# Performance work log

Measured on AMD Instinct MI355X. Metric: run time of the kernel, lower is better.

## Reference

```python
import jax, jax.numpy as jnp
import numpy as np

B, T, D, H = 256, 256, 384, 64  # batch, seq (BLOCK_SIZE), D_MODEL, HEAD_SIZE


def setup_inputs() -> dict:
    key = jax.random.key(0)
    k1, k2, k3, k4 = jax.random.split(key, 4)
    x = jax.random.normal(k1, (B, T, D), dtype=jnp.float32)
    # nn.Linear(D, H, bias=False): weight [H, D]; we store transposed [D, H] for x @ W
    Wq = jax.random.normal(k2, (D, H), dtype=jnp.float32) * (1.0 / np.sqrt(D))
    Wk = jax.random.normal(k3, (D, H), dtype=jnp.float32) * (1.0 / np.sqrt(D))
    Wv = jax.random.normal(k4, (D, H), dtype=jnp.float32) * (1.0 / np.sqrt(D))
    return {"x": x, "Wq": Wq, "Wk": Wk, "Wv": Wv}


def reference(x, Wq, Wk, Wv):
    # x: [B, T, D]
    q = x @ Wq  # [B, T, H]
    k = x @ Wk  # [B, T, H]
    v = x @ Wv  # [B, T, H]
    scale = 1.0 / jnp.sqrt(jnp.asarray(k.shape[-1], dtype=x.dtype))
    wei = jnp.einsum('bth,bsh->bts', q, k) * scale  # [B, T, T]
    causal = jnp.tril(jnp.ones((x.shape[1], x.shape[1]), dtype=bool))
    wei = jnp.where(causal, wei, -jnp.inf)
    wei = jax.nn.softmax(wei, axis=-1)
    # dropout is identity in eval mode (deterministic reference)
    out = jnp.einsum('bts,bsh->bth', wei, v)  # [B, T, H]
    return out
```

## Files before the change

### kernel.cpp

```cpp
#include <hip/hip_runtime.h>

#define BATCH 256
#define TT 256
#define DD 384
#define HH 64
#define SCALE 0.125f
#define SHIFT 14.0f

typedef __attribute__((ext_vector_type(8))) short short8;
typedef __attribute__((ext_vector_type(4))) float floatx4;

#define KS_STRIDE 72
#define QS_STRIDE 72
#define VT_STRIDE 264
#define PS_STRIDE 40
#define WELEMS (3 * DD * HH)

__device__ __forceinline__ unsigned short f2bf(float f) {
    unsigned int u = __float_as_uint(f);
    u += 0x7fffu + ((u >> 16) & 1u);
    return (unsigned short)(u >> 16);
}
__device__ __forceinline__ float bf2f(unsigned short u) {
    return __uint_as_float(((unsigned int)u) << 16);
}

__device__ __forceinline__ void gld_lds16(const void* g, void* ldst) {
    __builtin_amdgcn_global_load_lds(
        (__attribute__((address_space(1))) void*)(unsigned long long)g,
        (__attribute__((address_space(3))) void*)(unsigned int)(unsigned long long)ldst,
        16, 0, 0);
}

__device__ __forceinline__ short8 cvt8(float4 f0, float4 f1) {
    short8 a;
    a[0] = (short)f2bf(f0.x); a[1] = (short)f2bf(f0.y);
    a[2] = (short)f2bf(f0.z); a[3] = (short)f2bf(f0.w);
    a[4] = (short)f2bf(f1.x); a[5] = (short)f2bf(f1.y);
    a[6] = (short)f2bf(f1.z); a[7] = (short)f2bf(f1.w);
    return a;
}

__global__ void pack_w_kernel(const float* __restrict__ wq,
                              const float* __restrict__ wk,
                              const float* __restrict__ wv,
                              unsigned short* __restrict__ wf) {
    int idx = blockIdx.x * 256 + threadIdx.x;
    if (idx >= WELEMS) return;
    int j = idx & 7;
    int lane = (idx >> 3) & 63;
    int nt = (idx >> 9) & 3;
    int rem = idx >> 11;
    int mat = rem % 3;
    int ch = rem / 3;
    int l16 = lane & 15, q = lane >> 4;
    int h = 16 * nt + l16;
    int d = 32 * ch + 4 * q + (j < 4 ? j : j + 12);
    const float* w = (mat == 0) ? wq : (mat == 1) ? wk : wv;
    wf[idx] = f2bf(w[d * HH + h]);
}

__global__ __launch_bounds__(512, 2)
void fused_kernel(const float* __restrict__ x, const unsigned short* __restrict__ wfrag,
                  float* __restrict__ out) {
    __shared__ __align__(16) union LdsU {
        unsigned short w[WELEMS];
        struct {
            unsigned short ks[TT * KS_STRIDE];
            unsigned short vt[HH * VT_STRIDE];
            unsigned short q[TT * QS_STRIDE];
            unsigned short p[8][16 * PS_STRIDE];
        } s;
    } U;

    const int b = blockIdx.x;
    const int tid = threadIdx.x;
    const int wave = tid >> 6;
    const int lane = tid & 63;
    const int quad = lane >> 4;
    const int l16 = lane & 15;

    const float* xb = x + (size_t)b * TT * DD;

    const float* xr0 = xb + (size_t)(32 * wave + l16) * DD + 4 * quad;
    const float* xr1 = xr0 + (size_t)16 * DD;

    floatx4 cq[2][4] = {};
    floatx4 ck[2][4] = {};
    floatx4 cv[2][4] = {};

    float4 xP0_0, xP0_1, xP0_2, xP0_3;
    float4 xP1_0, xP1_1, xP1_2, xP1_3;
    float4 xP2_0, xP2_1, xP2_2, xP2_3;
    float4 xP3_0, xP3_1, xP3_2, xP3_3;

    #define XLOAD(B, CH)                                   \
        B##_0 = *(const float4*)(xr0 + (CH) * 32);         \
        B##_1 = *(const float4*)(xr0 + (CH) * 32 + 16);    \
        B##_2 = *(const float4*)(xr1 + (CH) * 32);         \
        B##_3 = *(const float4*)(xr1 + (CH) * 32 + 16);

    XLOAD(xP0, 0)
    XLOAD(xP1, 1)
    XLOAD(xP2, 2)
    XLOAD(xP3, 3)

    #pragma unroll
    for (int t = 0; t < 18; ++t) {
        int grp = wave * 18 + t;
        gld_lds16(wfrag + (size_t)grp * 512 + lane * 8, U.w + grp * 512);
    }

    __syncthreads();

    #define GEMM_BODY(B, CH)                                                       \
        {                                                                          \
            short8 a0 = cvt8(B##_0, B##_1);                                        \
            short8 a1 = cvt8(B##_2, B##_3);                                        \
            if ((CH) + 4 < 12) { XLOAD(B, (CH) + 4) }                              \
            const unsigned short* wb = U.w + (size_t)(CH) * 12 * 512 + lane * 8;   \
            short8 wf_[12];                                                        \
            _Pragma("unroll")                                                      \
            for (int i = 0; i < 12; ++i)                                           \
                wf_[i] = *(const short8*)(wb + (size_t)i * 512);                   \
            _Pragma("unroll")                                                      \
            for (int nt = 0; nt < 4; ++nt) {                                       \
                cq[0][nt] = __builtin_amdgcn_mfma_f32_16x16x32_bf16(a0, wf_[nt], cq[0][nt], 0, 0, 0);      \
                cq[1][nt] = __builtin_amdgcn_mfma_f32_16x16x32_bf16(a1, wf_[nt], cq[1][nt], 0, 0, 0);      \
                ck[0][nt] = __builtin_amdgcn_mfma_f32_16x16x32_bf16(a0, wf_[4 + nt], ck[0][nt], 0, 0, 0);  \
                ck[1][nt] = __builtin_amdgcn_mfma_f32_16x16x32_bf16(a1, wf_[4 + nt], ck[1][nt], 0, 0, 0);  \
                cv[0][nt] = __builtin_amdgcn_mfma_f32_16x16x32_bf16(a0, wf_[8 + nt], cv[0][nt], 0, 0, 0);  \
                cv[1][nt] = __builtin_amdgcn_mfma_f32_16x16x32_bf16(a1, wf_[8 + nt], cv[1][nt], 0, 0, 0);  \
            }                                                                      \
        }

    GEMM_BODY(xP0, 0)
    GEMM_BODY(xP1, 1)
    GEMM_BODY(xP2, 2)
    GEMM_BODY(xP3, 3)
    GEMM_BODY(xP0, 4)
    GEMM_BODY(xP1, 5)
    GEMM_BODY(xP2, 6)
    GEMM_BODY(xP3, 7)
    GEMM_BODY(xP0, 8)
    GEMM_BODY(xP1, 9)
    GEMM_BODY(xP2, 10)
    GEMM_BODY(xP3, 11)
    #undef GEMM_BODY
    #undef XLOAD

    __syncthreads();

    #pragma unroll
    for (int mi = 0; mi < 2; ++mi)
      #pragma unroll
      for (int nt = 0; nt < 4; ++nt)
        #pragma unroll
        for (int r = 0; r < 4; ++r) {
            int row = 32 * wave + 16 * mi + 4 * quad + r;
            int col = 16 * nt + l16;
            U.s.q[row * QS_STRIDE + col] = f2bf(cq[mi][nt][r]);
            U.s.ks[row * KS_STRIDE + col] = f2bf(ck[mi][nt][r]);
            U.s.vt[col * VT_STRIDE + row] = f2bf(cv[mi][nt][r]);
        }

    __syncthreads();

    floatx4 o[2][4] = {};
    float l_run[2][4] = {{0.f, 0.f, 0.f, 0.f}, {0.f, 0.f, 0.f, 0.f}};
    unsigned short* psw = U.s.p[wave];

    #pragma unroll
    for (int gi = 0; gi < 2; ++gi) {
        int g = gi ? (15 - wave) : wave;
        int gr0 = 16 * g;
        short8 aq0 = *(const short8*)(U.s.q + (size_t)(gr0 + l16) * QS_STRIDE + quad * 8);
        short8 aq1 = *(const short8*)(U.s.q + (size_t)(gr0 + l16) * QS_STRIDE + 32 + quad * 8);
        int clast = g >> 1;
        for (int c = 0; c <= clast; ++c) {
            floatx4 s[2] = {};
            #pragma unroll
            for (int ni = 0; ni < 2; ++ni) {
                const unsigned short* kbase =
                    U.s.ks + (size_t)(32 * c + 16 * ni + l16) * KS_STRIDE + quad * 8;
                s[ni] = __builtin_amdgcn_mfma_f32_16x16x32_bf16(aq0, *(const short8*)(kbase), s[ni], 0, 0, 0);
                s[ni] = __builtin_amdgcn_mfma_f32_16x16x32_bf16(aq1, *(const short8*)(kbase + 32), s[ni], 0, 0, 0);
            }
            bool partial = (c == clast);
            #pragma unroll
            for (int r = 0; r < 4; ++r) {
                int row = gr0 + 4 * quad + r;
                float p0 = __expf(s[0][r] * SCALE - SHIFT);
                float p1 = __expf(s[1][r] * SCALE - SHIFT);
                if (partial) {
                    if (32 * c + l16 > row) p0 = 0.f;
                    if (32 * c + 16 + l16 > row) p1 = 0.f;
                }
                unsigned short b0 = f2bf(p0), b1 = f2bf(p1);
                l_run[gi][r] += bf2f(b0) + bf2f(b1);
                psw[(4 * quad + r) * PS_STRIDE + l16] = b0;
                psw[(4 * quad + r) * PS_STRIDE + 16 + l16] = b1;
            }
            short8 ap = *(const short8*)(psw + l16 * PS_STRIDE + quad * 8);
            #pragma unroll
            for (int nt = 0; nt < 4; ++nt) {
                short8 bv = *(const short8*)(U.s.vt + (size_t)(16 * nt + l16) * VT_STRIDE + 32 * c + quad * 8);
                o[gi][nt] = __builtin_amdgcn_mfma_f32_16x16x32_bf16(ap, bv, o[gi][nt], 0, 0, 0);
            }
        }
    }

    float* outb = out + (size_t)b * TT * HH;
    #pragma unroll
    for (int gi = 0; gi < 2; ++gi) {
        int g = gi ? (15 - wave) : wave;
        float linv[4];
        #pragma unroll
        for (int r = 0; r < 4; ++r) {
            float l = l_run[gi][r];
            l += __shfl_xor(l, 1);
            l += __shfl_xor(l, 2);
            l += __shfl_xor(l, 4);
            l += __shfl_xor(l, 8);
            linv[r] = 1.0f / l;
        }
        #pragma unroll
        for (int nt = 0; nt < 4; ++nt)
          #pragma unroll
          for (int r = 0; r < 4; ++r) {
            int row = 16 * g + 4 * quad + r;
            outb[(size_t)row * HH + 16 * nt + l16] = o[gi][nt][r] * linv[r];
          }
    }
}

extern "C" void kernel_launch(void* const* d_in, const int* in_sizes, int n_in,
                              void* d_out, int out_size, void* d_ws, size_t ws_size,
                              hipStream_t stream) {
    const float* x  = (const float*)d_in[0];
    const float* wq = (const float*)d_in[1];
    const float* wk = (const float*)d_in[2];
    const float* wv = (const float*)d_in[3];
    unsigned short* wf = (unsigned short*)d_ws;
    float* o = (float*)d_out;

    pack_w_kernel<<<(WELEMS + 255) / 256, 256, 0, stream>>>(wq, wk, wv, wf);
    fused_kernel<<<BATCH, 512, 0, stream>>>(x, wf, o);
}
```

Measured before the change: 171.2 us.

## Prefetch K/V fragments from LDS, use packed bf16 convert, and raise MFMA priority

Adds a register double-buffer that loads the next chunk's K and V fragments from LDS while the current chunk's MFMAs and softmax run, so LDS latency is hidden. Replaces the software round-to-nearest float-to-bf16 conversion with the hardware v_cvt_pk_bf16_f32 instruction, both in the input conversion and for the softmax probabilities. Wraps the MFMA groups in s_setprio to favour matrix issue across waves. The double buffer raises VGPR pressure, which could lower occupancy.

```diff
diff --git a/kernel.cpp b/kernel.cpp
--- a/kernel.cpp
+++ b/kernel.cpp
@@ -25,6 +25,12 @@
     return __uint_as_float(((unsigned int)u) << 16);
 }
 
+__device__ __forceinline__ unsigned int cvtpk(float a, float b) {
+    unsigned int r;
+    asm("v_cvt_pk_bf16_f32 %0, %1, %2" : "=v"(r) : "v"(a), "v"(b));
+    return r;
+}
+
 __device__ __forceinline__ void gld_lds16(const void* g, void* ldst) {
     __builtin_amdgcn_global_load_lds(
         (__attribute__((address_space(1))) void*)(unsigned long long)g,
@@ -33,12 +39,12 @@
 }
 
 __device__ __forceinline__ short8 cvt8(float4 f0, float4 f1) {
-    short8 a;
-    a[0] = (short)f2bf(f0.x); a[1] = (short)f2bf(f0.y);
-    a[2] = (short)f2bf(f0.z); a[3] = (short)f2bf(f0.w);
-    a[4] = (short)f2bf(f1.x); a[5] = (short)f2bf(f1.y);
-    a[6] = (short)f2bf(f1.z); a[7] = (short)f2bf(f1.w);
-    return a;
+    union { unsigned int u[4]; short8 s; } r;
+    r.u[0] = cvtpk(f0.x, f0.y);
+    r.u[1] = cvtpk(f0.z, f0.w);
+    r.u[2] = cvtpk(f1.x, f1.y);
+    r.u[3] = cvtpk(f1.z, f1.w);
+    return r.s;
 }
 
 __global__ void pack_w_kernel(const float* __restrict__ wq,
@@ -177,15 +183,35 @@
         short8 aq0 = *(const short8*)(U.s.q + (size_t)(gr0 + l16) * QS_STRIDE + quad * 8);
         short8 aq1 = *(const short8*)(U.s.q + (size_t)(gr0 + l16) * QS_STRIDE + 32 + quad * 8);
         int clast = g >> 1;
+
+        short8 kf[4], vf[4], kn[4], vn[4];
+
+        #define LOADKV(KD, VD, C)                                                          \
+            {                                                                              \
+                _Pragma("unroll")                                                          \
+                for (int ni = 0; ni < 2; ++ni) {                                           \
+                    const unsigned short* kb =                                             \
+                        U.s.ks + (size_t)(32 * (C) + 16 * ni + l16) * KS_STRIDE + quad * 8;\
+                    KD[2 * ni]     = *(const short8*)(kb);                                 \
+                    KD[2 * ni + 1] = *(const short8*)(kb + 32);                            \
+                }                                                                          \
+                _Pragma("unroll")                                                          \
+                for (int nt = 0; nt < 4; ++nt)                                             \
+                    VD[nt] = *(const short8*)(U.s.vt + (size_t)(16 * nt + l16) * VT_STRIDE \
+                                              + 32 * (C) + quad * 8);                      \
+            }
+
+        LOADKV(kf, vf, 0)
+
         for (int c = 0; c <= clast; ++c) {
+            if (c < clast) { LOADKV(kn, vn, c + 1) }
             floatx4 s[2] = {};
-            #pragma unroll
-            for (int ni = 0; ni < 2; ++ni) {
-                const unsigned short* kbase =
-                    U.s.ks + (size_t)(32 * c + 16 * ni + l16) * KS_STRIDE + quad * 8;
-                s[ni] = __builtin_amdgcn_mfma_f32_16x16x32_bf16(aq0, *(const short8*)(kbase), s[ni], 0, 0, 0);
-                s[ni] = __builtin_amdgcn_mfma_f32_16x16x32_bf16(aq1, *(const short8*)(kbase + 32), s[ni], 0, 0, 0);
-            }
+            __builtin_amdgcn_s_setprio(1);
+            s[0] = __builtin_amdgcn_mfma_f32_16x16x32_bf16(aq0, kf[0], s[0], 0, 0, 0);
+            s[0] = __builtin_amdgcn_mfma_f32_16x16x32_bf16(aq1, kf[1], s[0], 0, 0, 0);
+            s[1] = __builtin_amdgcn_mfma_f32_16x16x32_bf16(aq0, kf[2], s[1], 0, 0, 0);
+            s[1] = __builtin_amdgcn_mfma_f32_16x16x32_bf16(aq1, kf[3], s[1], 0, 0, 0);
+            __builtin_amdgcn_s_setprio(0);
             bool partial = (c == clast);
             #pragma unroll
             for (int r = 0; r < 4; ++r) {
@@ -196,18 +222,25 @@
                     if (32 * c + l16 > row) p0 = 0.f;
                     if (32 * c + 16 + l16 > row) p1 = 0.f;
                 }
-                unsigned short b0 = f2bf(p0), b1 = f2bf(p1);
+                unsigned int pk = cvtpk(p0, p1);
+                unsigned short b0 = (unsigned short)pk;
+                unsigned short b1 = (unsigned short)(pk >> 16);
                 l_run[gi][r] += bf2f(b0) + bf2f(b1);
                 psw[(4 * quad + r) * PS_STRIDE + l16] = b0;
                 psw[(4 * quad + r) * PS_STRIDE + 16 + l16] = b1;
             }
             short8 ap = *(const short8*)(psw + l16 * PS_STRIDE + quad * 8);
+            __builtin_amdgcn_s_setprio(1);
             #pragma unroll
-            for (int nt = 0; nt < 4; ++nt) {
-                short8 bv = *(const short8*)(U.s.vt + (size_t)(16 * nt + l16) * VT_STRIDE + 32 * c + quad * 8);
-                o[gi][nt] = __builtin_amdgcn_mfma_f32_16x16x32_bf16(ap, bv, o[gi][nt], 0, 0, 0);
+            for (int nt = 0; nt < 4; ++nt)
+                o[gi][nt] = __builtin_amdgcn_mfma_f32_16x16x32_bf16(ap, vf[nt], o[gi][nt], 0, 0, 0);
+            __builtin_amdgcn_s_setprio(0);
+            if (c < clast) {
+                #pragma unroll
+                for (int i = 0; i < 4; ++i) { kf[i] = kn[i]; vf[i] = vn[i]; }
             }
         }
+        #undef LOADKV
     }
 
     float* outb = out + (size_t)b * TT * HH;
```

New measurement: 167.6 us. -2.1%, faster.
